# Kernel optimization log

Measured on AMD Instinct MI355X. Metric: run time of the kernel, lower is better.

## Reference

```python
import jax, jax.numpy as jnp
import numpy as np

EMBED = 1024
HEAD = 64

def setup_inputs() -> dict:
    key = jax.random.key(0)
    k1, k2, k3, k4 = jax.random.split(key, 4)
    # Torch Linear weight layout: [out_features, in_features]; xavier_uniform init
    bound = float(np.sqrt(6.0 / (EMBED + HEAD)))
    embeddings = jax.random.normal(k1, (4, 4096, EMBED), dtype=jnp.float32)
    W_Q = jax.random.uniform(k2, (HEAD, EMBED), dtype=jnp.float32, minval=-bound, maxval=bound)
    W_K = jax.random.uniform(k3, (HEAD, EMBED), dtype=jnp.float32, minval=-bound, maxval=bound)
    W_V = jax.random.uniform(k4, (HEAD, EMBED), dtype=jnp.float32, minval=-bound, maxval=bound)
    return {"embeddings": embeddings, "W_Q": W_Q, "W_K": W_K, "W_V": W_V}

def reference(embeddings, W_Q, W_K, W_V):
    # embeddings: [B, S, E]; weights: [H, E] (torch Linear layout, y = x @ W.T)
    B, S, E = embeddings.shape
    H = W_Q.shape[0]
    Q = jnp.einsum('bse,he->bsh', embeddings, W_Q)
    K = jnp.einsum('bse,he->bsh', embeddings, W_K)
    V = jnp.einsum('bse,he->bsh', embeddings, W_V)
    scale = 1.0 / jnp.sqrt(jnp.float32(H))
    scores = jnp.einsum('bqh,bkh->bqk', Q, K) * scale  # [B, S, S]
    causal = jnp.tril(jnp.ones((S, S), dtype=bool))
    scores = jnp.where(causal, scores, -jnp.inf)
    attn = jax.nn.softmax(scores, axis=-1)
    # dropout (p=0.1) is identity at inference; omitted for determinism
    return jnp.einsum('bqk,bkh->bqh', attn, V)  # [B, S, H]
```

## Files before the change

kernel.cpp:

```cpp
#include <hip/hip_runtime.h>
#include <hip/hip_bf16.h>

#define EMBED 1024
#define SEQ   4096
#define NBATCH 4
#define HD    64
#define CH    8
#define NP    8

typedef __attribute__((ext_vector_type(8))) short s16x8;
typedef __attribute__((ext_vector_type(4))) float f32x4;
typedef __attribute__((ext_vector_type(4))) unsigned int u32x4;

__device__ __forceinline__ short f2bf(float f) {
    unsigned u = __builtin_bit_cast(unsigned, f);
    u += 0x7fffu + ((u >> 16) & 1u);
    return (short)(u >> 16);
}

typedef const unsigned int __attribute__((address_space(1)))* gbl_ptr_t;
typedef unsigned int __attribute__((address_space(3)))* lds_ptr_t;
__device__ __forceinline__ void async16(const void* g, void* l) {
    __builtin_amdgcn_global_load_lds((gbl_ptr_t)g, (lds_ptr_t)l, 16, 0, 0);
}

__global__ __launch_bounds__(256) void prep_w(
    const float* __restrict__ wq, const float* __restrict__ wk,
    const float* __restrict__ wv, short* __restrict__ Wb)
{
    int idx = blockIdx.x * 256 + threadIdx.x;
    int e = idx * 8;
    int row = e >> 10, col = e & 1023;
    const float* src = (row < 64) ? (wq + (size_t)row * EMBED)
                     : (row < 128) ? (wk + (size_t)(row - 64) * EMBED)
                                   : (wv + (size_t)(row - 128) * EMBED);
    float sc = (row < 64) ? 0.125f : 1.0f;
    float4 f0 = *(const float4*)(src + col);
    float4 f1 = *(const float4*)(src + col + 4);
    s16x8 v = { f2bf(f0.x*sc), f2bf(f0.y*sc), f2bf(f0.z*sc), f2bf(f0.w*sc),
                f2bf(f1.x*sc), f2bf(f1.y*sc), f2bf(f1.z*sc), f2bf(f1.w*sc) };
    *(s16x8*)&Wb[e] = v;
}

__global__ __launch_bounds__(256) void proj_qkv(
    const float* __restrict__ emb, const short* __restrict__ Wb,
    short* __restrict__ Qb, short* __restrict__ Kb, short* __restrict__ Vt)
{
    __shared__ short Alds[2][32 * 64];
    __shared__ short Blds[2][192 * 64];

    const int tid  = threadIdx.x;
    const int lane = tid & 63;
    const int w    = tid >> 6;
    const int wr   = w & 1;
    const int wc   = w >> 1;
    const int row0 = blockIdx.x * 32;

    const int sr   = tid >> 3;
    const int sg   = tid & 7;
    const int srow = lane >> 3;
    const int sblk = lane & 7;

    f32x4 acc[6];
#pragma unroll
    for (int i = 0; i < 6; ++i) acc[i] = f32x4{0.f, 0.f, 0.f, 0.f};

    auto stageB = [&](int buf, int t) {
        const int k0 = t * 64;
#pragma unroll
        for (int i = 0; i < 6; ++i) {
            int r = w * 48 + i * 8 + srow;
            async16(Wb + (size_t)r * EMBED + k0 + ((sblk ^ (r & 7)) * 8),
                    &Blds[buf][(w * 48 + i * 8) * 64]);
        }
    };
    const float* abase = emb + (size_t)(row0 + sr) * EMBED + sg * 8;
    auto writeA = [&](int buf, float4 f0, float4 f1) {
        s16x8 v = { f2bf(f0.x), f2bf(f0.y), f2bf(f0.z), f2bf(f0.w),
                    f2bf(f1.x), f2bf(f1.y), f2bf(f1.z), f2bf(f1.w) };
        *(s16x8*)&Alds[buf][sr * 64 + ((sg ^ (sr & 7)) * 8)] = v;
    };

    float4 f0a = *(const float4*)(abase);
    float4 f1a = *(const float4*)(abase + 4);
    stageB(0, 0);
    writeA(0, f0a, f1a);
    f0a = *(const float4*)(abase + 64);
    f1a = *(const float4*)(abase + 68);
    stageB(1, 1);
    asm volatile("s_waitcnt vmcnt(8) lgkmcnt(0)" ::: "memory");
    __builtin_amdgcn_s_barrier();
    __builtin_amdgcn_sched_barrier(0);

    int cur = 0;
    const int ar = wr * 16 + (lane & 15);
    const int ag = lane >> 4;

    for (int t = 0; t < 16; ++t) {
        s16x8 a0 = *(const s16x8*)&Alds[cur][ar * 64 + (((ag    ) ^ (ar & 7)) * 8)];
        s16x8 a1 = *(const s16x8*)&Alds[cur][ar * 64 + (((ag + 4) ^ (ar & 7)) * 8)];
#pragma unroll
        for (int n = 0; n < 6; ++n) {
            int br = wc * 96 + n * 16 + (lane & 15);
            s16x8 b0 = *(const s16x8*)&Blds[cur][br * 64 + (((ag    ) ^ (br & 7)) * 8)];
            s16x8 b1 = *(const s16x8*)&Blds[cur][br * 64 + (((ag + 4) ^ (br & 7)) * 8)];
            acc[n] = __builtin_amdgcn_mfma_f32_16x16x32_bf16(a0, b0, acc[n], 0, 0, 0);
            acc[n] = __builtin_amdgcn_mfma_f32_16x16x32_bf16(a1, b1, acc[n], 0, 0, 0);
        }
        if (t == 15) break;

        __builtin_amdgcn_s_barrier();
        __builtin_amdgcn_sched_barrier(0);
        writeA(cur ^ 1, f0a, f1a);
        if (t < 14) {
            f0a = *(const float4*)(abase + (size_t)(t + 2) * 64);
            f1a = *(const float4*)(abase + (size_t)(t + 2) * 64 + 4);
            stageB(cur, t + 2);
            asm volatile("s_waitcnt vmcnt(8) lgkmcnt(0)" ::: "memory");
        } else {
            asm volatile("s_waitcnt vmcnt(0) lgkmcnt(0)" ::: "memory");
        }
        __builtin_amdgcn_s_barrier();
        __builtin_amdgcn_sched_barrier(0);
        cur ^= 1;
    }

    const int rbase = row0 + wr * 16 + ((lane >> 4) * 4);
    const int cl = lane & 15;
#pragma unroll
    for (int n = 0; n < 6; ++n) {
        int col = wc * 96 + n * 16 + cl;
        int mat = col >> 6;
        int c = col & 63;
#pragma unroll
        for (int r = 0; r < 4; ++r) {
            int row = rbase + r;
            int b = row >> 12, s = row & 4095;
            short v = f2bf(acc[n][r]);
            if (mat == 0)       Qb[((size_t)b * SEQ + s) * HD + c] = v;
            else if (mat == 1)  Kb[((size_t)b * SEQ + s) * HD + c] = v;
            else                Vt[((size_t)b * HD + c) * SEQ + s] = v;
        }
    }
}

__global__ __launch_bounds__(256) void attn_fwd(
    const short* __restrict__ Qb, const short* __restrict__ Kb,
    const short* __restrict__ Vt, float* __restrict__ Op, float* __restrict__ Ml)
{
    const int b = blockIdx.y;
    const int i = 287 - blockIdx.x;
    int k = (int)((sqrtf((float)(16 + 16 * i)) - 4.0f) * 0.125f);
    while (4 * (k + 1) * (k + 2) <= i) ++k;
    while (4 * k * (k + 1) > i) --k;
    const int rem = i - 4 * k * (k + 1);
    const int kp1 = k + 1;
    const int jq = 8 * k + rem / kp1;
    const int p  = rem - (rem / kp1) * kp1;
    const int t0 = p * CH;
    const int t1 = min(t0 + CH, jq + 1);

    __shared__ short Klds[2][64 * 64];
    __shared__ short Vlds[2][64 * 64];

    const int tid  = threadIdx.x;
    const int lane = tid & 63;
    const int w    = tid >> 6;
    const int l15  = lane & 15;
    const int g    = lane >> 4;
    const int q0w  = jq * 64 + w * 16;

    const short* Kbase0 = Kb + (size_t)b * SEQ * HD;
    const short* Vbase0 = Vt + (size_t)b * HD * SEQ;

    const int srow = lane >> 3;
    const int sblk = lane & 7;

    auto stageKV = [&](int buf, int t) {
        const int kv0 = t * 64;
#pragma unroll
        for (int i2 = 0; i2 < 2; ++i2) {
            int r = w * 16 + i2 * 8 + srow;
            async16(Kbase0 + (size_t)(kv0 + r) * HD + ((sblk ^ (r & 7)) * 8),
                    &Klds[buf][(w * 16 + i2 * 8) * 64]);
            async16(Vbase0 + (size_t)r * SEQ + kv0 + ((sblk ^ (r & 7)) * 8),
                    &Vlds[buf][(w * 16 + i2 * 8) * 64]);
        }
    };

    const short* qp = Qb + ((size_t)b * SEQ + q0w + l15) * HD + g * 8;
    s16x8 qb0 = *(const s16x8*)qp;
    s16x8 qb1 = *(const s16x8*)(qp + 32);

    stageKV(0, t0);
    if (t0 + 1 < t1) {
        stageKV(1, t0 + 1);
        asm volatile("s_waitcnt vmcnt(4)" ::: "memory");
    } else {
        asm volatile("s_waitcnt vmcnt(0)" ::: "memory");
    }
    __builtin_amdgcn_s_barrier();
    __builtin_amdgcn_sched_barrier(0);

    f32x4 o[4];
#pragma unroll
    for (int n = 0; n < 4; ++n) o[n] = f32x4{0.f, 0.f, 0.f, 0.f};
    float m = -INFINITY, l = 0.f;

    const int f1l = (2 * (g & 1) + (g >> 1)) * 16 + l15;
    const int f2l = (2 * (g & 1) + 1 - (g >> 1)) * 16 + l15;
    const bool podd = (g & 1) != 0;
    const bool hbit = (g >> 1) != 0;

    int cur = 0;
    for (int t = t0; t < t1; ++t) {
        f32x4 st[4];
        __builtin_amdgcn_s_setprio(1);
#pragma unroll
        for (int n = 0; n < 4; ++n) {
            int kr = n * 16 + l15;
            s16x8 ka0 = *(const s16x8*)&Klds[cur][kr * 64 + (((g    ) ^ (kr & 7)) * 8)];
            s16x8 ka1 = *(const s16x8*)&Klds[cur][kr * 64 + (((g + 4) ^ (kr & 7)) * 8)];
            st[n] = __builtin_amdgcn_mfma_f32_16x16x32_bf16(ka0, qb0, f32x4{0.f,0.f,0.f,0.f}, 0, 0, 0);
            st[n] = __builtin_amdgcn_mfma_f32_16x16x32_bf16(ka1, qb1, st[n], 0, 0, 0);
        }
        __builtin_amdgcn_s_setprio(0);

        if (t == jq) {
#pragma unroll
            for (int n = 0; n < 4; ++n)
#pragma unroll
                for (int r = 0; r < 4; ++r) {
                    int kvg = t * 64 + n * 16 + g * 4 + r;
                    if (kvg > q0w + l15) st[n][r] = -INFINITY;
                }
        }

        float mt = fmaxf(fmaxf(st[0][0], st[0][1]), fmaxf(st[0][2], st[0][3]));
#pragma unroll
        for (int n = 1; n < 4; ++n)
            mt = fmaxf(mt, fmaxf(fmaxf(st[n][0], st[n][1]), fmaxf(st[n][2], st[n][3])));
        mt = fmaxf(mt, __shfl_xor(mt, 16, 64));
        mt = fmaxf(mt, __shfl_xor(mt, 32, 64));

        if (__any(mt - m > 8.f)) {
            float mn  = fmaxf(m, mt);
            float fac = __expf(m - mn);
            m = mn;
            l *= fac;
#pragma unroll
            for (int n = 0; n < 4; ++n)
#pragma unroll
                for (int r = 0; r < 4; ++r) o[n][r] *= fac;
        }

        float rs = 0.f;
        unsigned pk[4][2];
#pragma unroll
        for (int n = 0; n < 4; ++n) {
            float p0 = __expf(st[n][0] - m);
            float p1 = __expf(st[n][1] - m);
            float p2 = __expf(st[n][2] - m);
            float p3 = __expf(st[n][3] - m);
            rs += (p0 + p1) + (p2 + p3);
            asm("v_cvt_pk_bf16_f32 %0, %1, %2" : "=v"(pk[n][0]) : "v"(p0), "v"(p1));
            asm("v_cvt_pk_bf16_f32 %0, %1, %2" : "=v"(pk[n][1]) : "v"(p2), "v"(p3));
        }
        rs += __shfl_xor(rs, 16, 64);
        rs += __shfl_xor(rs, 32, 64);
        l += rs;

        __builtin_amdgcn_s_setprio(1);
#pragma unroll
        for (int kk = 0; kk < 2; ++kk) {
            unsigned e00 = podd ? pk[2 * kk + 1][0] : pk[2 * kk][0];
            unsigned e01 = podd ? pk[2 * kk + 1][1] : pk[2 * kk][1];
            unsigned e10 = podd ? pk[2 * kk][0]     : pk[2 * kk + 1][0];
            unsigned e11 = podd ? pk[2 * kk][1]     : pk[2 * kk + 1][1];
            unsigned x0 = (unsigned)__shfl((int)e00, f1l, 64);
            unsigned x1 = (unsigned)__shfl((int)e01, f1l, 64);
            unsigned y0 = (unsigned)__shfl((int)e10, f2l, 64);
            unsigned y1 = (unsigned)__shfl((int)e11, f2l, 64);
            unsigned w0 = hbit ? y0 : x0;
            unsigned w1 = hbit ? y1 : x1;
            unsigned w2 = hbit ? x0 : y0;
            unsigned w3 = hbit ? x1 : y1;
            u32x4 uu = { w0, w1, w2, w3 };
            s16x8 pb = __builtin_bit_cast(s16x8, uu);
#pragma unroll
            for (int n = 0; n < 4; ++n) {
                int vr = n * 16 + l15;
                s16x8 va = *(const s16x8*)&Vlds[cur][vr * 64 + (((g + kk * 4) ^ (vr & 7)) * 8)];
                o[n] = __builtin_amdgcn_mfma_f32_16x16x32_bf16(va, pb, o[n], 0, 0, 0);
            }
        }
        __builtin_amdgcn_s_setprio(0);

        if (t + 1 < t1) {
            __builtin_amdgcn_s_barrier();
            __builtin_amdgcn_sched_barrier(0);
            if (t + 2 < t1) {
                stageKV(cur, t + 2);
                asm volatile("s_waitcnt vmcnt(4)" ::: "memory");
            } else {
                asm volatile("s_waitcnt vmcnt(0)" ::: "memory");
            }
            __builtin_amdgcn_s_barrier();
            __builtin_amdgcn_sched_barrier(0);
            cur ^= 1;
        }
    }

    const size_t pidx = ((size_t)b * 64 + jq) * NP + p;
    float* opb = Op + pidx * 4096;
#pragma unroll
    for (int n = 0; n < 4; ++n)
#pragma unroll
        for (int r = 0; r < 4; ++r)
            opb[(n * 16 + g * 4 + r) * 64 + w * 16 + l15] = o[n][r];
    if (lane < 16) {
        float* mlb = Ml + pidx * 128;
        mlb[w * 16 + l15]      = m;
        mlb[64 + w * 16 + l15] = l;
    }
}

__global__ __launch_bounds__(256) void attn_combine(
    const float* __restrict__ Op, const float* __restrict__ Ml,
    float* __restrict__ out)
{
    const int jq = blockIdx.x;
    const int b  = blockIdx.y;
    const int nP = (jq >> 3) + 1;
    const int tid = threadIdx.x;
    const int q  = tid & 63;
    const int dc = tid >> 6;
    const size_t pb = ((size_t)b * 64 + jq) * NP;

    float mv[NP], lv[NP], wt[NP];
    float mstar = -INFINITY;
#pragma unroll
    for (int p = 0; p < NP; ++p) if (p < nP) {
        mv[p] = Ml[(pb + p) * 128 + q];
        lv[p] = Ml[(pb + p) * 128 + 64 + q];
        mstar = fmaxf(mstar, mv[p]);
    }
    float L = 0.f;
#pragma unroll
    for (int p = 0; p < NP; ++p) if (p < nP) {
        wt[p] = __expf(mv[p] - mstar);
        L += lv[p] * wt[p];
    }
    float inv = 1.0f / L;

    float acc[16];
#pragma unroll
    for (int k2 = 0; k2 < 16; ++k2) acc[k2] = 0.f;
#pragma unroll
    for (int p = 0; p < NP; ++p) if (p < nP) {
        const float* src = Op + (pb + p) * 4096 + (size_t)dc * 16 * 64 + q;
#pragma unroll
        for (int k2 = 0; k2 < 16; ++k2) acc[k2] += src[k2 * 64] * wt[p];
    }
    float* dst = out + ((size_t)b * SEQ + jq * 64 + q) * HD + dc * 16;
#pragma unroll
    for (int k2 = 0; k2 < 16; ++k2) dst[k2] = acc[k2] * inv;
}

extern "C" void kernel_launch(void* const* d_in, const int* in_sizes, int n_in,
                              void* d_out, int out_size, void* d_ws, size_t ws_size,
                              hipStream_t stream)
{
    (void)in_sizes; (void)n_in; (void)out_size; (void)ws_size;
    const float* emb = (const float*)d_in[0];
    const float* wq  = (const float*)d_in[1];
    const float* wk  = (const float*)d_in[2];
    const float* wv  = (const float*)d_in[3];
    float* out = (float*)d_out;

    short* Wb = (short*)d_ws;
    short* Qb = Wb + 192 * 1024;
    short* Kb = Qb + (size_t)NBATCH * SEQ * HD;
    short* Vt = Kb + (size_t)NBATCH * SEQ * HD;
    float* Op = (float*)(Vt + (size_t)NBATCH * SEQ * HD);
    float* Ml = Op + (size_t)NBATCH * 64 * NP * 64 * 64;

    hipLaunchKernelGGL(prep_w, dim3(96), dim3(256), 0, stream, wq, wk, wv, Wb);
    hipLaunchKernelGGL(proj_qkv, dim3(512), dim3(256), 0, stream, emb, Wb, Qb, Kb, Vt);
    hipLaunchKernelGGL(attn_fwd, dim3(288, NBATCH), dim3(256), 0, stream,
                       Qb, Kb, Vt, Op, Ml);
    hipLaunchKernelGGL(attn_combine, dim3(64, NBATCH), dim3(256), 0, stream,
                       Op, Ml, out);
}
```

Before: 150.3 us.

## Double attention query tile to 128 rows with 512-thread blocks, drop sched barriers

Measured after the change: 149.1 us. Within noise of the previous version (-0.8%).

```diff
diff --git a/kernel.cpp b/kernel.cpp
--- a/kernel.cpp
+++ b/kernel.cpp
@@ -23,6 +23,7 @@
 __device__ __forceinline__ void async16(const void* g, void* l) {
     __builtin_amdgcn_global_load_lds((gbl_ptr_t)g, (lds_ptr_t)l, 16, 0, 0);
 }
+#define MEMFENCE asm volatile("" ::: "memory")
 
 __global__ __launch_bounds__(256) void prep_w(
     const float* __restrict__ wq, const float* __restrict__ wk,
@@ -90,7 +91,7 @@
     stageB(1, 1);
     asm volatile("s_waitcnt vmcnt(8) lgkmcnt(0)" ::: "memory");
     __builtin_amdgcn_s_barrier();
-    __builtin_amdgcn_sched_barrier(0);
+    MEMFENCE;
 
     int cur = 0;
     const int ar = wr * 16 + (lane & 15);
@@ -110,7 +111,7 @@
         if (t == 15) break;
 
         __builtin_amdgcn_s_barrier();
-        __builtin_amdgcn_sched_barrier(0);
+        MEMFENCE;
         writeA(cur ^ 1, f0a, f1a);
         if (t < 14) {
             f0a = *(const float4*)(abase + (size_t)(t + 2) * 64);
@@ -121,7 +122,7 @@
             asm volatile("s_waitcnt vmcnt(0) lgkmcnt(0)" ::: "memory");
         }
         __builtin_amdgcn_s_barrier();
-        __builtin_amdgcn_sched_barrier(0);
+        MEMFENCE;
         cur ^= 1;
     }
 
@@ -144,21 +145,22 @@
     }
 }
 
-__global__ __launch_bounds__(256) void attn_fwd(
+__global__ __launch_bounds__(512) void attn_fwd(
     const short* __restrict__ Qb, const short* __restrict__ Kb,
     const short* __restrict__ Vt, float* __restrict__ Op, float* __restrict__ Ml)
 {
     const int b = blockIdx.y;
-    const int i = 287 - blockIdx.x;
-    int k = (int)((sqrtf((float)(16 + 16 * i)) - 4.0f) * 0.125f);
-    while (4 * (k + 1) * (k + 2) <= i) ++k;
-    while (4 * k * (k + 1) > i) --k;
-    const int rem = i - 4 * k * (k + 1);
-    const int kp1 = k + 1;
-    const int jq = 8 * k + rem / kp1;
-    const int p  = rem - (rem / kp1) * kp1;
-    const int t0 = p * CH;
-    const int t1 = min(t0 + CH, jq + 1);
+    const int i = 143 - blockIdx.x;
+    int a = (int)((sqrtf((float)(1 + 2 * i)) - 1.0f) * 0.5f);
+    while (2 * (a + 1) * (a + 2) <= i) ++a;
+    while (2 * a * (a + 1) > i) --a;
+    const int rem = i - 2 * a * (a + 1);
+    const int ap1 = a + 1;
+    const int r_  = rem / ap1;
+    const int jq  = 4 * a + r_;
+    const int p   = rem - r_ * ap1;
+    const int t0  = p * CH;
+    const int t1  = min(t0 + CH, 2 * jq + 2);
 
     __shared__ short Klds[2][64 * 64];
     __shared__ short Vlds[2][64 * 64];
@@ -168,7 +170,7 @@
     const int w    = tid >> 6;
     const int l15  = lane & 15;
     const int g    = lane >> 4;
-    const int q0w  = jq * 64 + w * 16;
+    const int q0w  = jq * 128 + w * 16;
 
     const short* Kbase0 = Kb + (size_t)b * SEQ * HD;
     const short* Vbase0 = Vt + (size_t)b * HD * SEQ;
@@ -178,14 +180,11 @@
 
     auto stageKV = [&](int buf, int t) {
         const int kv0 = t * 64;
-#pragma unroll
-        for (int i2 = 0; i2 < 2; ++i2) {
-            int r = w * 16 + i2 * 8 + srow;
-            async16(Kbase0 + (size_t)(kv0 + r) * HD + ((sblk ^ (r & 7)) * 8),
-                    &Klds[buf][(w * 16 + i2 * 8) * 64]);
-            async16(Vbase0 + (size_t)r * SEQ + kv0 + ((sblk ^ (r & 7)) * 8),
-                    &Vlds[buf][(w * 16 + i2 * 8) * 64]);
-        }
+        int r = w * 8 + srow;
+        async16(Kbase0 + (size_t)(kv0 + r) * HD + ((sblk ^ (r & 7)) * 8),
+                &Klds[buf][(w * 8) * 64]);
+        async16(Vbase0 + (size_t)r * SEQ + kv0 + ((sblk ^ (r & 7)) * 8),
+                &Vlds[buf][(w * 8) * 64]);
     };
 
     const short* qp = Qb + ((size_t)b * SEQ + q0w + l15) * HD + g * 8;
@@ -195,12 +194,12 @@
     stageKV(0, t0);
     if (t0 + 1 < t1) {
         stageKV(1, t0 + 1);
-        asm volatile("s_waitcnt vmcnt(4)" ::: "memory");
+        asm volatile("s_waitcnt vmcnt(2)" ::: "memory");
     } else {
         asm volatile("s_waitcnt vmcnt(0)" ::: "memory");
     }
     __builtin_amdgcn_s_barrier();
-    __builtin_amdgcn_sched_barrier(0);
+    MEMFENCE;
 
     f32x4 o[4];
 #pragma unroll
@@ -226,13 +225,13 @@
         }
         __builtin_amdgcn_s_setprio(0);
 
-        if (t == jq) {
+        if (t * 64 + 63 > q0w) {
 #pragma unroll
             for (int n = 0; n < 4; ++n)
 #pragma unroll
-                for (int r = 0; r < 4; ++r) {
-                    int kvg = t * 64 + n * 16 + g * 4 + r;
-                    if (kvg > q0w + l15) st[n][r] = -INFINITY;
+                for (int r2 = 0; r2 < 4; ++r2) {
+                    int kvg = t * 64 + n * 16 + g * 4 + r2;
+                    if (kvg > q0w + l15) st[n][r2] = -INFINITY;
                 }
         }
 
@@ -251,7 +250,7 @@
 #pragma unroll
             for (int n = 0; n < 4; ++n)
 #pragma unroll
-                for (int r = 0; r < 4; ++r) o[n][r] *= fac;
+                for (int r2 = 0; r2 < 4; ++r2) o[n][r2] *= fac;
         }
 
         float rs = 0.f;
@@ -298,30 +297,30 @@
 
         if (t + 1 < t1) {
             __builtin_amdgcn_s_barrier();
-            __builtin_amdgcn_sched_barrier(0);
+            MEMFENCE;
             if (t + 2 < t1) {
                 stageKV(cur, t + 2);
-                asm volatile("s_waitcnt vmcnt(4)" ::: "memory");
+                asm volatile("s_waitcnt vmcnt(2)" ::: "memory");
             } else {
                 asm volatile("s_waitcnt vmcnt(0)" ::: "memory");
             }
             __builtin_amdgcn_s_barrier();
-            __builtin_amdgcn_sched_barrier(0);
+            MEMFENCE;
             cur ^= 1;
         }
     }
 
-    const size_t pidx = ((size_t)b * 64 + jq) * NP + p;
-    float* opb = Op + pidx * 4096;
+    const size_t pidx = ((size_t)b * 32 + jq) * NP + p;
+    float* opb = Op + pidx * 8192;
 #pragma unroll
     for (int n = 0; n < 4; ++n)
 #pragma unroll
-        for (int r = 0; r < 4; ++r)
-            opb[(n * 16 + g * 4 + r) * 64 + w * 16 + l15] = o[n][r];
+        for (int r2 = 0; r2 < 4; ++r2)
+            opb[(n * 16 + g * 4 + r2) * 128 + w * 16 + l15] = o[n][r2];
     if (lane < 16) {
-        float* mlb = Ml + pidx * 128;
-        mlb[w * 16 + l15]      = m;
-        mlb[64 + w * 16 + l15] = l;
+        float* mlb = Ml + pidx * 256;
+        mlb[w * 16 + l15]       = m;
+        mlb[128 + w * 16 + l15] = l;
     }
 }
 
@@ -331,18 +330,18 @@
 {
     const int jq = blockIdx.x;
     const int b  = blockIdx.y;
-    const int nP = (jq >> 3) + 1;
+    const int nP = (jq >> 2) + 1;
     const int tid = threadIdx.x;
-    const int q  = tid & 63;
-    const int dc = tid >> 6;
-    const size_t pb = ((size_t)b * 64 + jq) * NP;
+    const int q  = tid & 127;
+    const int dc = tid >> 7;
+    const size_t pb = ((size_t)b * 32 + jq) * NP;
 
     float mv[NP], lv[NP], wt[NP];
     float mstar = -INFINITY;
 #pragma unroll
     for (int p = 0; p < NP; ++p) if (p < nP) {
-        mv[p] = Ml[(pb + p) * 128 + q];
-        lv[p] = Ml[(pb + p) * 128 + 64 + q];
+        mv[p] = Ml[(pb + p) * 256 + q];
+        lv[p] = Ml[(pb + p) * 256 + 128 + q];
         mstar = fmaxf(mstar, mv[p]);
     }
     float L = 0.f;
@@ -353,18 +352,18 @@
     }
     float inv = 1.0f / L;
 
-    float acc[16];
-#pragma unroll
-    for (int k2 = 0; k2 < 16; ++k2) acc[k2] = 0.f;
+    float acc[32];
+#pragma unroll
+    for (int k2 = 0; k2 < 32; ++k2) acc[k2] = 0.f;
 #pragma unroll
     for (int p = 0; p < NP; ++p) if (p < nP) {
-        const float* src = Op + (pb + p) * 4096 + (size_t)dc * 16 * 64 + q;
-#pragma unroll
-        for (int k2 = 0; k2 < 16; ++k2) acc[k2] += src[k2 * 64] * wt[p];
-    }
-    float* dst = out + ((size_t)b * SEQ + jq * 64 + q) * HD + dc * 16;
-#pragma unroll
-    for (int k2 = 0; k2 < 16; ++k2) dst[k2] = acc[k2] * inv;
+        const float* src = Op + (pb + p) * 8192 + (size_t)dc * 32 * 128 + q;
+#pragma unroll
+        for (int k2 = 0; k2 < 32; ++k2) acc[k2] += src[k2 * 128] * wt[p];
+    }
+    float* dst = out + ((size_t)b * SEQ + jq * 128 + q) * HD + dc * 32;
+#pragma unroll
+    for (int k2 = 0; k2 < 32; ++k2) dst[k2] = acc[k2] * inv;
 }
 
 extern "C" void kernel_launch(void* const* d_in, const int* in_sizes, int n_in,
@@ -383,12 +382,12 @@
     short* Kb = Qb + (size_t)NBATCH * SEQ * HD;
     short* Vt = Kb + (size_t)NBATCH * SEQ * HD;
     float* Op = (float*)(Vt + (size_t)NBATCH * SEQ * HD);
-    float* Ml = Op + (size_t)NBATCH * 64 * NP * 64 * 64;
+    float* Ml = Op + (size_t)NBATCH * 32 * NP * 8192;
 
     hipLaunchKernelGGL(prep_w, dim3(96), dim3(256), 0, stream, wq, wk, wv, Wb);
     hipLaunchKernelGGL(proj_qkv, dim3(512), dim3(256), 0, stream, emb, Wb, Qb, Kb, Vt);
-    hipLaunchKernelGGL(attn_fwd, dim3(288, NBATCH), dim3(256), 0, stream,
+    hipLaunchKernelGGL(attn_fwd, dim3(144, NBATCH), dim3(512), 0, stream,
                        Qb, Kb, Vt, Op, Ml);
-    hipLaunchKernelGGL(attn_combine, dim3(64, NBATCH), dim3(256), 0, stream,
+    hipLaunchKernelGGL(attn_combine, dim3(32, NBATCH), dim3(256), 0, stream,
                        Op, Ml, out);
 }
```
